# Kernel tuning notes

Measured on AMD Instinct MI355X. Metric: run time of the kernel, lower is better.

## Reference

```python
import jax, jax.numpy as jnp
import numpy as np

# ---- static part graph (matches torch.nonzero row-major edge order) ----
ADJ = np.array([[0,1,0,0,0,0],
                [1,0,1,1,1,1],
                [0,1,0,0,0,0],
                [0,1,0,0,0,0],
                [0,1,0,0,0,1],
                [0,1,0,0,1,0]], dtype=np.int64)
EDGES = [(int(u), int(v)) for u, v in np.argwhere(ADJ)]  # 12 edges
P = ADJ.shape[0]                 # 6 part nodes (cls_p - 1)
PART_LIST = [[] for _ in range(P)]
for u, v in EDGES:
    PART_LIST[v].append(u)
DEG = [len(l) for l in PART_LIST]  # [1,5,1,1,2,2], sum = 12
CLS_P = P + 1
IN_DIM, HID = 256, 10
N, H, W = 4, 64, 64


def spatial_coords(h, w):
    """[8,h,w] coord features, same as generate_spatial_batch (vectorized)."""
    ws = np.arange(w, dtype=np.float32); hs = np.arange(h, dtype=np.float32)
    xmin = ws / w * 2 - 1; xmax = (ws + 1) / w * 2 - 1; xctr = (xmin + xmax) / 2
    ymin = hs / h * 2 - 1; ymax = (hs + 1) / h * 2 - 1; yctr = (ymin + ymax) / 2
    f = np.zeros((h, w, 8), np.float32)
    f[..., 0] = xmin[None, :]; f[..., 1] = ymin[:, None]
    f[..., 2] = xmax[None, :]; f[..., 3] = ymax[:, None]
    f[..., 4] = xctr[None, :]; f[..., 5] = yctr[:, None]
    f[..., 6] = 1.0 / w;       f[..., 7] = 1.0 / h
    return jnp.asarray(f.transpose(2, 0, 1))


def conv1x1(x, w, b=None):
    y = jnp.einsum('nchw,oc->nohw', x, w)
    return y if b is None else y + b[None, :, None, None]


def conv3x3(x, w):
    return jax.lax.conv_general_dilated(x, w, (1, 1), 'SAME',
                                        dimension_numbers=('NCHW', 'OIHW', 'NCHW'))


def bn(x, g, b, eps=1e-5):
    mu = x.mean((0, 2, 3), keepdims=True)
    var = ((x - mu) ** 2).mean((0, 2, 3), keepdims=True)
    return (x - mu) * jax.lax.rsqrt(var + eps) * g[None, :, None, None] + b[None, :, None, None]


def setup_inputs() -> dict:
    key = jax.random.key(0)
    ks = jax.random.split(key, 16)
    s = 0.05
    return {
        'xp':      jax.random.normal(ks[0], (N, IN_DIM, H, W), jnp.float32),
        'p_nodes': jax.random.normal(ks[1], (CLS_P, N, HID, H, W), jnp.float32),
        'p_atts':  jax.random.normal(ks[2], (CLS_P, N, 1, H, W), jnp.float32),
        'W_key':  jax.random.normal(ks[3], (64, IN_DIM + 8), jnp.float32) * s,
        'b_key':  jnp.zeros((64,), jnp.float32),
        'W_q':    jax.random.normal(ks[4], (64, IN_DIM + 8), jnp.float32) * s,
        'b_q':    jnp.zeros((64,), jnp.float32),
        'W_att':  jax.random.normal(ks[5], (sum(DEG), IN_DIM + 1), jnp.float32) * s,
        'b_att':  jnp.zeros((sum(DEG),), jnp.float32),
        'W_proj': jax.random.normal(ks[6], (HID, IN_DIM), jnp.float32) * s,
        'g_proj': jnp.ones((HID,), jnp.float32),
        'bt_proj': jnp.zeros((HID,), jnp.float32),
        'W_rel1': jax.random.normal(ks[7], (2 * HID, 2 * HID, 3, 3), jnp.float32) * s,
        'g_rel1': jnp.ones((2 * HID,), jnp.float32),
        'bt_rel1': jnp.zeros((2 * HID,), jnp.float32),
        'W_rel2': jax.random.normal(ks[8], (HID, 2 * HID), jnp.float32) * s,
        'b_rel2': jnp.zeros((HID,), jnp.float32),
        'Wg':    jax.random.normal(ks[9], (P, 2, 2 * HID), jnp.float32) * s,
        'bg':    jnp.zeros((P, 2), jnp.float32),
        'Wc':    jax.random.normal(ks[10], (P, HID, 2 * HID), jnp.float32) * s,
        'g_can': jnp.ones((P, HID), jnp.float32),
        'bt_can': jnp.zeros((P, HID), jnp.float32),
    }


def reference(xp, p_nodes, p_atts,
              W_key, b_key, W_q, b_q, W_att, b_att,
              W_proj, g_proj, bt_proj, W_rel1, g_rel1, bt_rel1, W_rel2, b_rel2,
              Wg, bg, Wc, g_can, bt_can):
    n, c, h, w = xp.shape
    L = h * w
    coord = jnp.broadcast_to(spatial_coords(h, w), (n, 8, h, w))

    # ---- Dep_Context (vectorized over the P part nodes) ----
    feat = jnp.concatenate([xp, coord], axis=1)                 # [n, 264, h, w]
    key_f = conv1x1(feat, W_key, b_key).reshape(n, 64, L)       # [n, 64, L]
    p_att = p_atts[1:]                                          # [P, n, 1, h, w]
    norm = jax.nn.softmax(p_att.reshape(P, n, L), axis=-1)      # [P, n, L]
    hu_c = jnp.einsum('ncl,pnl->pnc', xp.reshape(n, c, L), norm)       # [P, n, 256]
    co_c = jnp.einsum('ncl,pnl->pnc', coord.reshape(n, 8, L), norm)    # [P, n, 8]
    cen = jnp.concatenate([hu_c, co_c], axis=-1)                # [P, n, 264]
    q = jnp.einsum('pnf,of->pno', cen, W_q) + b_q               # [P, n, 64]
    energy = jnp.einsum('pno,nol->pnl', q, key_f)               # [P, n, L]
    attn = jax.nn.sigmoid(energy).reshape(P, n, 1, h, w)
    one_m = 1.0 - p_att
    F_dep_att = attn * one_m                                    # [P, n, 1, h, w]
    F_dep = attn * xp[None] * one_m                             # [P, n, 256, h, w]

    # ---- Contexture attention heads (per-node conv, deg_i output channels) ----
    att_logits, att_soft = [], []
    off = 0
    for i in range(P):
        d = DEG[i]
        inp = jnp.concatenate([F_dep_att[i], xp], axis=1)       # [n, 257, h, w]
        logit = conv1x1(inp, W_att[off:off + d], b_att[off:off + d])
        att_logits.append(logit)
        att_soft.append(jax.nn.softmax(logit, axis=1))
        off += d

    # ---- Dependency messages per edge ----
    def dependency(hv, hu_ctx, dep_att):
        msg = jax.nn.relu(bn(conv1x1(hu_ctx * dep_att, W_proj), g_proj, bt_proj))
        x = jnp.concatenate([msg, hv], axis=1)                  # [n, 20, h, w]
        x = jax.nn.relu(bn(conv3x3(x, W_rel1), g_rel1, bt_rel1))
        return jax.nn.sigmoid(conv1x1(x, W_rel2, b_rel2))       # [n, 10, h, w]

    msgs = [None] * P
    for u, v in EDGES:
        ch = PART_LIST[u].index(v)
        # NB: original code indexes p_node_list with the raw edge target v
        m = dependency(p_nodes[v], F_dep[u], att_soft[u][:, ch:ch + 1])
        msgs[v] = m if msgs[v] is None else msgs[v] + m

    # ---- ConvGRU node updates ----
    new_nodes = [p_nodes[0]]
    for i in range(P):
        h_cur, msg = p_nodes[i + 1], msgs[i]
        gates = conv1x1(jnp.concatenate([msg, h_cur], axis=1), Wg[i], bg[i])
        r = jax.nn.sigmoid(gates[:, 0:1]); z = jax.nn.sigmoid(gates[:, 1:2])
        cnm = conv1x1(jnp.concatenate([msg, r * h_cur], axis=1), Wc[i])
        cnm = jax.nn.leaky_relu(bn(cnm, g_can[i], bt_can[i]), 0.01)  # InPlaceABNSync default
        new_nodes.append((1.0 - z) * h_cur + z * cnm)

    xp_new = jnp.stack(new_nodes)                               # [cls_p, n, 10, h, w]
    fdep_att = jnp.concatenate(att_logits, axis=1)              # [n, 12, h, w]
    return xp_new, fdep_att
```

## Files before the change

### kernel.cpp

```cpp
#include <hip/hip_runtime.h>
#include <math.h>

#define L 4096

__constant__ int c_EV[12]   = {1,0,2,3,4,5,1,1,1,5,1,4};
__constant__ int c_INOFF[7] = {0,1,6,7,8,10,12};
__constant__ int c_INE[12]  = {1, 0,6,7,8,10, 2, 3, 4,11, 5,9};

__device__ inline float sigmf(float x){ return 1.f/(1.f+expf(-x)); }

__global__ __launch_bounds__(256) void k_softmax_norm(const float* __restrict__ p_atts,
                                                      float* __restrict__ norm){
  int pn = blockIdx.x;
  const float* src = p_atts + (size_t)(pn + 4) * L;
  float* dst = norm + (size_t)pn * L;
  __shared__ float red[256];
  int tid = threadIdx.x;
  float m = -1e30f;
  for (int l = tid; l < L; l += 256) m = fmaxf(m, src[l]);
  red[tid] = m; __syncthreads();
  for (int s = 128; s; s >>= 1){ if (tid < s) red[tid] = fmaxf(red[tid], red[tid+s]); __syncthreads(); }
  m = red[0]; __syncthreads();
  float sum = 0.f;
  for (int l = tid; l < L; l += 256) sum += expf(src[l] - m);
  red[tid] = sum; __syncthreads();
  for (int s = 128; s; s >>= 1){ if (tid < s) red[tid] += red[tid+s]; __syncthreads(); }
  float inv = 1.f / red[0];
  for (int l = tid; l < L; l += 256) dst[l] = expf(src[l] - m) * inv;
}

__device__ inline float coord_feat(int cc, int l){
  int h = l >> 6, w = l & 63;
  const float s = 2.f / 64.f;
  switch (cc){
    case 0: return w * s - 1.f;
    case 1: return h * s - 1.f;
    case 2: return (w + 1) * s - 1.f;
    case 3: return (h + 1) * s - 1.f;
    case 4: return (w + 0.5f) * s - 1.f;
    case 5: return (h + 0.5f) * s - 1.f;
    default: return 1.f / 64.f;
  }
}

__global__ __launch_bounds__(256) void k_centroid(const float* __restrict__ xp,
                                                  const float* __restrict__ norm,
                                                  float* __restrict__ cen){
  int c = blockIdx.x;
  int n = blockIdx.y;
  int tid = threadIdx.x;
  float acc[6];
#pragma unroll
  for (int p = 0; p < 6; p++) acc[p] = 0.f;
  const float* nr0 = norm + (size_t)n * L;
  if (c < 256){
    const float* xr = xp + ((size_t)n * 256 + c) * L;
    for (int l = tid; l < L; l += 256){
      float xv = xr[l];
#pragma unroll
      for (int p = 0; p < 6; p++) acc[p] = fmaf(xv, nr0[(size_t)p * 4 * L + l], acc[p]);
    }
  } else {
    int cc = c - 256;
    for (int l = tid; l < L; l += 256){
      float xv = coord_feat(cc, l);
#pragma unroll
      for (int p = 0; p < 6; p++) acc[p] = fmaf(xv, nr0[(size_t)p * 4 * L + l], acc[p]);
    }
  }
#pragma unroll
  for (int p = 0; p < 6; p++){
    for (int off = 32; off; off >>= 1) acc[p] += __shfl_xor(acc[p], off, 64);
  }
  __shared__ float red[6][4];
  int wv = tid >> 6;
  if ((tid & 63) == 0){
#pragma unroll
    for (int p = 0; p < 6; p++) red[p][wv] = acc[p];
  }
  __syncthreads();
  if (tid < 6){
    float s = red[tid][0] + red[tid][1] + red[tid][2] + red[tid][3];
    cen[(size_t)(tid * 4 + n) * 264 + c] = s;
  }
}

__global__ __launch_bounds__(256) void k_qk(const float* __restrict__ cen,
                                            const float* __restrict__ W_q, const float* __restrict__ b_q,
                                            const float* __restrict__ W_key, const float* __restrict__ b_key,
                                            float* __restrict__ qk, float* __restrict__ qb){
  int pn = blockIdx.x;
  int tid = threadIdx.x;
  __shared__ float cen_s[264];
  __shared__ float qs[64];
  __shared__ float part[256];
  for (int i = tid; i < 264; i += 256) cen_s[i] = cen[(size_t)pn * 264 + i];
  __syncthreads();
  int o = tid >> 2, pr = tid & 3;
  {
    float a = 0.f;
    int f0 = pr * 66;
    for (int j = 0; j < 66; j++){ int f = f0 + j; a = fmaf(cen_s[f], W_q[o * 264 + f], a); }
    part[tid] = a;
  }
  __syncthreads();
  if (pr == 0) qs[o] = part[tid] + part[tid + 1] + part[tid + 2] + part[tid + 3] + b_q[o];
  __syncthreads();
  for (int c = tid; c < 264; c += 256){
    float a = 0.f;
    for (int oo = 0; oo < 64; oo++) a = fmaf(qs[oo], W_key[oo * 264 + c], a);
    qk[(size_t)pn * 264 + c] = a;
  }
  if (tid < 64) part[tid] = qs[tid] * b_key[tid];
  __syncthreads();
  if (tid == 0){
    float a = 0.f;
    for (int oo = 0; oo < 64; oo++) a += part[oo];
    qb[pn] = a;
  }
}

__global__ __launch_bounds__(256) void k_wt(const float* __restrict__ W_rel1, float* __restrict__ wt2){
  for (int i = threadIdx.x; i < 3600; i += 256){
    int co = i % 10; int t = i / 10;
    int k = t % 9; t /= 9;
    int h = t & 1; int ci = t >> 1;
    wt2[i] = W_rel1[(((h * 10 + co) * 20) + ci) * 9 + k];
  }
}

__global__ __launch_bounds__(256) void k_pixel(const float* __restrict__ xp,
                                              const float* __restrict__ p_atts,
                                              const float* __restrict__ W_att, const float* __restrict__ b_att,
                                              const float* __restrict__ W_proj,
                                              const float* __restrict__ qk, const float* __restrict__ qb,
                                              float* __restrict__ out_fdep,
                                              float* __restrict__ s_edge,
                                              float* __restrict__ proj_x){
  __shared__ float s_watt[256 * 12];
  __shared__ float s_wproj[256 * 12];
  __shared__ float s_qk[256 * 8];
  __shared__ float s_qkt[48];
  __shared__ float pacc[4][28][64];
  __shared__ float w0[12], ba[12], qbs[6];
  int n = blockIdx.y;
  int tid = threadIdx.x;
  int wv = tid >> 6, w = tid & 63;
  int l = blockIdx.x * 64 + w;
  for (int i = tid; i < 256 * 12; i += 256){ int c = i / 12, j = i % 12; s_watt[i] = W_att[j * 257 + 1 + c]; }
  for (int i = tid; i < 256 * 12; i += 256){ int c = i / 12, k = i % 12; s_wproj[i] = (k < 10) ? W_proj[k * 256 + c] : 0.f; }
  for (int i = tid; i < 256 * 8; i += 256){ int c = i >> 3, p = i & 7; s_qk[i] = (p < 6) ? qk[((size_t)(p * 4 + n)) * 264 + c] : 0.f; }
  if (tid < 48){ int p = tid >> 3, cc = tid & 7; s_qkt[tid] = qk[((size_t)(p * 4 + n)) * 264 + 256 + cc]; }
  if (tid < 12){ w0[tid] = W_att[tid * 257]; ba[tid] = b_att[tid]; }
  if (tid < 6) qbs[tid] = qb[tid * 4 + n];
  __syncthreads();

  float a[32];
#pragma unroll
  for (int f = 0; f < 32; f++) a[f] = 0.f;
  const float* xpn = xp + (size_t)n * 256 * L + l;
  int c0 = wv * 64;
#pragma unroll 2
  for (int cc = 0; cc < 64; cc++){
    int c = c0 + cc;
    float xv = xpn[(size_t)c * L];
    float4 wa0 = *(const float4*)(s_watt + c * 12);
    float4 wa1 = *(const float4*)(s_watt + c * 12 + 4);
    float4 wa2 = *(const float4*)(s_watt + c * 12 + 8);
    float4 wp0 = *(const float4*)(s_wproj + c * 12);
    float4 wp1 = *(const float4*)(s_wproj + c * 12 + 4);
    float4 wp2 = *(const float4*)(s_wproj + c * 12 + 8);
    float4 wq0 = *(const float4*)(s_qk + c * 8);
    float4 wq1 = *(const float4*)(s_qk + c * 8 + 4);
    a[0]  = fmaf(xv, wa0.x, a[0]);  a[1]  = fmaf(xv, wa0.y, a[1]);
    a[2]  = fmaf(xv, wa0.z, a[2]);  a[3]  = fmaf(xv, wa0.w, a[3]);
    a[4]  = fmaf(xv, wa1.x, a[4]);  a[5]  = fmaf(xv, wa1.y, a[5]);
    a[6]  = fmaf(xv, wa1.z, a[6]);  a[7]  = fmaf(xv, wa1.w, a[7]);
    a[8]  = fmaf(xv, wa2.x, a[8]);  a[9]  = fmaf(xv, wa2.y, a[9]);
    a[10] = fmaf(xv, wa2.z, a[10]); a[11] = fmaf(xv, wa2.w, a[11]);
    a[12] = fmaf(xv, wp0.x, a[12]); a[13] = fmaf(xv, wp0.y, a[13]);
    a[14] = fmaf(xv, wp0.z, a[14]); a[15] = fmaf(xv, wp0.w, a[15]);
    a[16] = fmaf(xv, wp1.x, a[16]); a[17] = fmaf(xv, wp1.y, a[17]);
    a[18] = fmaf(xv, wp1.z, a[18]); a[19] = fmaf(xv, wp1.w, a[19]);
    a[20] = fmaf(xv, wp2.x, a[20]); a[21] = fmaf(xv, wp2.y, a[21]);
    a[24] = fmaf(xv, wq0.x, a[24]); a[25] = fmaf(xv, wq0.y, a[25]);
    a[26] = fmaf(xv, wq0.z, a[26]); a[27] = fmaf(xv, wq0.w, a[27]);
    a[28] = fmaf(xv, wq1.x, a[28]); a[29] = fmaf(xv, wq1.y, a[29]);
  }
#pragma unroll
  for (int f = 0; f < 12; f++) pacc[wv][f][w] = a[f];
#pragma unroll
  for (int k = 0; k < 10; k++) pacc[wv][12 + k][w] = a[12 + k];
#pragma unroll
  for (int p = 0; p < 6; p++) pacc[wv][22 + p][w] = a[24 + p];
  __syncthreads();
  for (int idx = tid; idx < 28 * 64; idx += 256){
    int f = idx >> 6, ww = idx & 63;
    pacc[0][f][ww] = pacc[0][f][ww] + pacc[1][f][ww] + pacc[2][f][ww] + pacc[3][f][ww];
  }
  __syncthreads();
  if (tid < 64){
    float accA[12], accP[10], accE[6];
#pragma unroll
    for (int j = 0; j < 12; j++) accA[j] = pacc[0][j][w];
#pragma unroll
    for (int k = 0; k < 10; k++) accP[k] = pacc[0][12 + k][w];
#pragma unroll
    for (int p = 0; p < 6; p++) accE[p] = pacc[0][22 + p][w];

    float cf[8];
    { int hh = l >> 6, ww2 = l & 63; const float s = 2.f / 64.f;
      cf[0] = ww2 * s - 1.f; cf[1] = hh * s - 1.f; cf[2] = (ww2 + 1) * s - 1.f; cf[3] = (hh + 1) * s - 1.f;
      cf[4] = (ww2 + 0.5f) * s - 1.f; cf[5] = (hh + 0.5f) * s - 1.f; cf[6] = 1.f / 64.f; cf[7] = 1.f / 64.f; }
    float sat[6];
#pragma unroll
    for (int p = 0; p < 6; p++){
      float e = accE[p] + qbs[p];
#pragma unroll
      for (int cc = 0; cc < 8; cc++) e = fmaf(cf[cc], s_qkt[p * 8 + cc], e);
      float aa = sigmf(e);
      float pa = p_atts[((size_t)(p + 1) * 4 + n) * L + l];
      sat[p] = aa * (1.f - pa);
    }
    const int part_of[12] = {0,1,1,1,1,1,2,3,4,4,5,5};
    float lg[12];
#pragma unroll
    for (int j = 0; j < 12; j++){
      lg[j] = accA[j] + w0[j] * sat[part_of[j]] + ba[j];
      out_fdep[((size_t)n * 12 + j) * L + l] = lg[j];
    }
    const int gs[6] = {0,1,6,7,8,10}, gd[6] = {1,5,1,1,2,2};
    float sm[12];
#pragma unroll
    for (int g = 0; g < 6; g++){
      int s0 = gs[g], d = gd[g];
      float mx = lg[s0];
      for (int t = 1; t < d; t++) mx = fmaxf(mx, lg[s0 + t]);
      float ssum = 0.f;
      for (int t = 0; t < d; t++){ float e2 = expf(lg[s0 + t] - mx); sm[s0 + t] = e2; ssum += e2; }
      float inv = 1.f / ssum;
      for (int t = 0; t < d; t++) sm[s0 + t] *= inv;
    }
#pragma unroll
    for (int e = 0; e < 12; e++) s_edge[((size_t)e * 4 + n) * L + l] = sat[part_of[e]] * sm[e];
#pragma unroll
    for (int k = 0; k < 10; k++) proj_x[((size_t)n * 10 + k) * L + l] = accP[k];
  }
}

__global__ __launch_bounds__(256) void k_msg_stats(const float* __restrict__ proj_x,
                                                   const float* __restrict__ s_edge,
                                                   float* __restrict__ mu, float* __restrict__ istd){
  int e = blockIdx.x / 10, k = blockIdx.x % 10;
  int tid = threadIdx.x;
  float s1 = 0.f, s2 = 0.f;
  for (int idx = tid; idx < 4 * L; idx += 256){
    int n = idx >> 12, l = idx & (L - 1);
    float t = proj_x[((size_t)n * 10 + k) * L + l] * s_edge[((size_t)e * 4 + n) * L + l];
    s1 += t; s2 += t * t;
  }
  __shared__ float r1[256], r2[256];
  r1[tid] = s1; r2[tid] = s2; __syncthreads();
  for (int s = 128; s; s >>= 1){ if (tid < s){ r1[tid] += r1[tid+s]; r2[tid] += r2[tid+s]; } __syncthreads(); }
  if (tid == 0){
    float m = r1[0] / 16384.f, v = r2[0] / 16384.f - m * m;
    mu[blockIdx.x] = m; istd[blockIdx.x] = rsqrtf(v + 1e-5f);
  }
}

__global__ __launch_bounds__(256) void k_conv3(const float* __restrict__ proj_x,
                                               const float* __restrict__ s_edge,
                                               const float* __restrict__ mu, const float* __restrict__ istd,
                                               const float* __restrict__ g_proj, const float* __restrict__ bt_proj,
                                               const float* __restrict__ p_nodes,
                                               const float* __restrict__ wt2,
                                               float* __restrict__ y,
                                               float* __restrict__ ypart){
  __shared__ float red[4][20];
  int rb = blockIdx.x, n = blockIdx.y;
  int e = blockIdx.z >> 1, h = blockIdx.z & 1;
  int v = c_EV[e];
  int tid = threadIdx.x;
  int wv = tid >> 6, w = tid & 63;
  int row = rb * 4 + wv;
  float mLm = (w == 0) ? 0.f : 1.f;
  float mRm = (w == 63) ? 0.f : 1.f;

  float scs[10], sbs[10];
#pragma unroll
  for (int k = 0; k < 10; k++){
    int ek = e * 10 + k;
    float s = istd[ek] * g_proj[k];
    scs[k] = s; sbs[k] = bt_proj[k] - mu[ek] * s;
  }
  const size_t enL = ((size_t)e * 4 + n) * L;
  const float* se = s_edge + enL;

  float acc[10];
#pragma unroll
  for (int co = 0; co < 10; co++) acc[co] = 0.f;

#pragma unroll 2
  for (int ci = 0; ci < 10; ci++){
    const float* pr = proj_x + ((size_t)n * 10 + ci) * L;
    float a = 0.f, b, c = 0.f;
    { int pix = row * 64 + w; float t = pr[pix] * se[pix]; b = fmaxf(fmaf(t, scs[ci], sbs[ci]), 0.f); }
    if (row > 0){ int pix = (row - 1) * 64 + w; float t = pr[pix] * se[pix]; a = fmaxf(fmaf(t, scs[ci], sbs[ci]), 0.f); }
    if (row < 63){ int pix = (row + 1) * 64 + w; float t = pr[pix] * se[pix]; c = fmaxf(fmaf(t, scs[ci], sbs[ci]), 0.f); }
    float aL = __shfl_up(a, 1) * mLm;
    float aR = __shfl_down(a, 1) * mRm;
    float bL = __shfl_up(b, 1) * mLm;
    float bR = __shfl_down(b, 1) * mRm;
    float cL = __shfl_up(c, 1) * mLm;
    float cR = __shfl_down(c, 1) * mRm;
    const float* wp = wt2 + (ci * 2 + h) * 90;
#pragma unroll
    for (int co = 0; co < 10; co++){
      float s0 = fmaf(aL, wp[co], fmaf(a, wp[10 + co], aR * wp[20 + co]));
      s0 = fmaf(bL, wp[30 + co], fmaf(b, wp[40 + co], fmaf(bR, wp[50 + co], s0)));
      s0 = fmaf(cL, wp[60 + co], fmaf(c, wp[70 + co], fmaf(cR, wp[80 + co], s0)));
      acc[co] += s0;
    }
  }
#pragma unroll 2
  for (int ci = 10; ci < 20; ci++){
    const float* pn = p_nodes + (((size_t)v * 4 + n) * 10 + (ci - 10)) * L;
    float a = 0.f, b, c = 0.f;
    b = pn[row * 64 + w];
    if (row > 0)  a = pn[(row - 1) * 64 + w];
    if (row < 63) c = pn[(row + 1) * 64 + w];
    float aL = __shfl_up(a, 1) * mLm;
    float aR = __shfl_down(a, 1) * mRm;
    float bL = __shfl_up(b, 1) * mLm;
    float bR = __shfl_down(b, 1) * mRm;
    float cL = __shfl_up(c, 1) * mLm;
    float cR = __shfl_down(c, 1) * mRm;
    const float* wp = wt2 + (ci * 2 + h) * 90;
#pragma unroll
    for (int co = 0; co < 10; co++){
      float s0 = fmaf(aL, wp[co], fmaf(a, wp[10 + co], aR * wp[20 + co]));
      s0 = fmaf(bL, wp[30 + co], fmaf(b, wp[40 + co], fmaf(bR, wp[50 + co], s0)));
      s0 = fmaf(cL, wp[60 + co], fmaf(c, wp[70 + co], fmaf(cR, wp[80 + co], s0)));
      acc[co] += s0;
    }
  }

  int ch0 = h * 10;
#pragma unroll
  for (int co = 0; co < 10; co++)
    y[(enL * 20) + ((size_t)(ch0 + co)) * L + row * 64 + w] = acc[co];

#pragma unroll
  for (int co = 0; co < 10; co++){
    float s1 = acc[co];
    float s2 = acc[co] * acc[co];
    for (int off = 32; off; off >>= 1){ s1 += __shfl_xor(s1, off, 64); s2 += __shfl_xor(s2, off, 64); }
    if (w == 0){ red[wv][2 * co] = s1; red[wv][2 * co + 1] = s2; }
  }
  __syncthreads();
  if (tid < 20){
    int co = tid >> 1, which = tid & 1;
    float s = red[0][tid] + red[1][tid] + red[2][tid] + red[3][tid];
    ypart[(((size_t)(e * 20 + ch0 + co) * 64) + n * 16 + rb) * 2 + which] = s;
  }
}

__global__ __launch_bounds__(64) void k_red(const float* __restrict__ part,
                                            float* __restrict__ mu, float* __restrict__ istd){
  int ent = blockIdx.x;
  int t = threadIdx.x;
  const float* p = part + ((size_t)ent * 64 + t) * 2;
  float s1 = p[0], s2 = p[1];
  for (int off = 32; off; off >>= 1){ s1 += __shfl_xor(s1, off, 64); s2 += __shfl_xor(s2, off, 64); }
  if (t == 0){
    float m = s1 / 16384.f, v = s2 / 16384.f - m * m;
    mu[ent] = m; istd[ent] = rsqrtf(v + 1e-5f);
  }
}

__global__ __launch_bounds__(256) void k_mout_gru(const float* __restrict__ y,
                                                  const float* __restrict__ mu_y, const float* __restrict__ istd_y,
                                                  const float* __restrict__ g_rel1, const float* __restrict__ bt_rel1,
                                                  const float* __restrict__ W_rel2, const float* __restrict__ b_rel2,
                                                  const float* __restrict__ p_nodes,
                                                  const float* __restrict__ Wg, const float* __restrict__ bg,
                                                  const float* __restrict__ Wc,
                                                  float* __restrict__ cnm, float* __restrict__ zbuf,
                                                  float* __restrict__ cpart){
  int i = blockIdx.z, n = blockIdx.y;
  int tid = threadIdx.x;
  int l = blockIdx.x * 256 + tid;
  __shared__ float w2[200], wc[200], wg[40], bgs[2];
  __shared__ float sc[5][20], sb[5][20];
  __shared__ float red[4][20];
  int ne = c_INOFF[i + 1] - c_INOFF[i];
  for (int t = tid; t < 200; t += 256){ w2[t] = W_rel2[t]; wc[t] = Wc[i * 200 + t]; }
  if (tid < 40) wg[tid] = Wg[i * 40 + tid];
  if (tid < 2) bgs[tid] = bg[i * 2 + tid];
  if (tid < ne * 20){
    int ei = tid / 20, c = tid % 20;
    int e = c_INE[c_INOFF[i] + ei];
    int ec = e * 20 + c;
    float s = istd_y[ec] * g_rel1[c];
    sc[ei][c] = s; sb[ei][c] = bt_rel1[c] - mu_y[ec] * s;
  }
  __syncthreads();
  float m[10];
#pragma unroll
  for (int k = 0; k < 10; k++) m[k] = 0.f;
  for (int ei = 0; ei < ne; ei++){
    int e = c_INE[c_INOFF[i] + ei];
    float z[20];
#pragma unroll
    for (int c = 0; c < 20; c++){
      float t = y[(((size_t)e * 4 + n) * 20 + c) * L + l];
      z[c] = fmaxf(t * sc[ei][c] + sb[ei][c], 0.f);
    }
#pragma unroll
    for (int k = 0; k < 10; k++){
      float a = b_rel2[k];
#pragma unroll
      for (int c = 0; c < 20; c++) a = fmaf(w2[k * 20 + c], z[c], a);
      m[k] += sigmf(a);
    }
  }
  float h[10];
#pragma unroll
  for (int k = 0; k < 10; k++) h[k] = p_nodes[(((size_t)(i + 1) * 4 + n) * 10 + k) * L + l];
  float g0 = bgs[0], g1 = bgs[1];
#pragma unroll
  for (int k = 0; k < 10; k++){
    g0 = fmaf(wg[k], m[k], g0); g0 = fmaf(wg[10 + k], h[k], g0);
    g1 = fmaf(wg[20 + k], m[k], g1); g1 = fmaf(wg[30 + k], h[k], g1);
  }
  float r = sigmf(g0), zz = sigmf(g1);
  zbuf[((size_t)i * 4 + n) * L + l] = zz;
  float cv[10];
#pragma unroll
  for (int k = 0; k < 10; k++){
    float a = 0.f;
#pragma unroll
    for (int c = 0; c < 10; c++){
      a = fmaf(wc[k * 20 + c], m[c], a);
      a = fmaf(wc[k * 20 + 10 + c], r * h[c], a);
    }
    cv[k] = a;
    cnm[(((size_t)i * 4 + n) * 10 + k) * L + l] = a;
  }
  int wv = tid >> 6, w = tid & 63;
#pragma unroll
  for (int k = 0; k < 10; k++){
    float s1 = cv[k], s2 = cv[k] * cv[k];
    for (int off = 32; off; off >>= 1){ s1 += __shfl_xor(s1, off, 64); s2 += __shfl_xor(s2, off, 64); }
    if (w == 0){ red[wv][2 * k] = s1; red[wv][2 * k + 1] = s2; }
  }
  __syncthreads();
  if (tid < 20){
    float s = red[0][tid] + red[1][tid] + red[2][tid] + red[3][tid];
    int k = tid >> 1, which = tid & 1;
    cpart[(((size_t)(i * 10 + k) * 64) + n * 16 + blockIdx.x) * 2 + which] = s;
  }
}

__global__ __launch_bounds__(256) void k_out(const float* __restrict__ cnm, const float* __restrict__ zbuf,
                                             const float* __restrict__ p_nodes,
                                             const float* __restrict__ mu, const float* __restrict__ istd,
                                             const float* __restrict__ g_can, const float* __restrict__ bt_can,
                                             float* __restrict__ out){
  int idx = blockIdx.x * 256 + threadIdx.x;
  const int NODE = 4 * 10 * L;
  if (idx < NODE){ out[idx] = p_nodes[idx]; return; }
  int j = idx - NODE;
  int l = j & (L - 1); int r = j >> 12;
  int k = r % 10; r /= 10; int n = r & 3; int i = r >> 2;
  int ik = i * 10 + k;
  float c = cnm[j];
  float cn = (c - mu[ik]) * istd[ik] * g_can[ik] + bt_can[ik];
  cn = cn > 0.f ? cn : 0.01f * cn;
  float z = zbuf[((size_t)i * 4 + n) * L + l];
  float h = p_nodes[idx];
  out[idx] = (1.f - z) * h + z * cn;
}

extern "C" void kernel_launch(void* const* d_in, const int* in_sizes, int n_in,
                              void* d_out, int out_size, void* d_ws, size_t ws_size,
                              hipStream_t stream){
  (void)in_sizes; (void)n_in; (void)out_size; (void)ws_size;
  const float* xp      = (const float*)d_in[0];
  const float* p_nodes = (const float*)d_in[1];
  const float* p_atts  = (const float*)d_in[2];
  const float* W_key   = (const float*)d_in[3];
  const float* b_key   = (const float*)d_in[4];
  const float* W_q     = (const float*)d_in[5];
  const float* b_q     = (const float*)d_in[6];
  const float* W_att   = (const float*)d_in[7];
  const float* b_att   = (const float*)d_in[8];
  const float* W_proj  = (const float*)d_in[9];
  const float* g_proj  = (const float*)d_in[10];
  const float* bt_proj = (const float*)d_in[11];
  const float* W_rel1  = (const float*)d_in[12];
  const float* g_rel1  = (const float*)d_in[13];
  const float* bt_rel1 = (const float*)d_in[14];
  const float* W_rel2  = (const float*)d_in[15];
  const float* b_rel2  = (const float*)d_in[16];
  const float* Wg      = (const float*)d_in[17];
  const float* bg      = (const float*)d_in[18];
  const float* Wc      = (const float*)d_in[19];
  const float* g_can   = (const float*)d_in[20];
  const float* bt_can  = (const float*)d_in[21];

  float* out      = (float*)d_out;
  float* fdep_out = out + (size_t)7 * 4 * 10 * L;

  float* w = (float*)d_ws;
  size_t off = 0;
  auto alloc = [&](size_t nf){ float* p = w + off; off += nf; return p; };
  float* norm    = alloc((size_t)6 * 4 * L);
  float* cen     = alloc(6 * 4 * 264);
  float* qk      = alloc(6 * 4 * 264);
  float* qb      = alloc(24);
  float* wt2     = alloc(3600);
  float* proj_x  = alloc((size_t)4 * 10 * L);
  float* s_edge  = alloc((size_t)12 * 4 * L);
  float* mu_msg  = alloc(120);
  float* istd_msg= alloc(120);
  float* ybuf    = alloc((size_t)12 * 4 * 20 * L);
  float* ypart   = alloc(240 * 64 * 2);
  float* cpart   = alloc(60 * 64 * 2);
  float* mu_y    = alloc(240);
  float* istd_y  = alloc(240);
  float* cnm     = alloc((size_t)6 * 4 * 10 * L);
  float* zbuf    = alloc((size_t)6 * 4 * L);
  float* mu_c    = alloc(60);
  float* istd_c  = alloc(60);

  k_wt<<<1, 256, 0, stream>>>(W_rel1, wt2);
  k_softmax_norm<<<24, 256, 0, stream>>>(p_atts, norm);
  { dim3 g(264, 4); k_centroid<<<g, 256, 0, stream>>>(xp, norm, cen); }
  k_qk<<<24, 256, 0, stream>>>(cen, W_q, b_q, W_key, b_key, qk, qb);
  { dim3 g(64, 4); k_pixel<<<g, 256, 0, stream>>>(xp, p_atts, W_att, b_att, W_proj, qk, qb, fdep_out, s_edge, proj_x); }
  k_msg_stats<<<120, 256, 0, stream>>>(proj_x, s_edge, mu_msg, istd_msg);
  { dim3 g(16, 4, 24); k_conv3<<<g, 256, 0, stream>>>(proj_x, s_edge, mu_msg, istd_msg, g_proj, bt_proj, p_nodes, wt2, ybuf, ypart); }
  k_red<<<240, 64, 0, stream>>>(ypart, mu_y, istd_y);
  { dim3 g(16, 4, 6); k_mout_gru<<<g, 256, 0, stream>>>(ybuf, mu_y, istd_y, g_rel1, bt_rel1, W_rel2, b_rel2,
                                                        p_nodes, Wg, bg, Wc, cnm, zbuf, cpart); }
  k_red<<<60, 64, 0, stream>>>(cpart, mu_c, istd_c);
  k_out<<<(7 * 4 * 10 * L) / 256, 256, 0, stream>>>(cnm, zbuf, p_nodes, mu_c, istd_c, g_can, bt_can, out);
}
```

Measured before the change: 162.8 us.

## Compute two output rows per thread in conv3 and fuse weight transpose kernel

The 3x3 conv kernel now has each thread produce two adjacent output rows, so it loads 4 input rows instead of 3 per output row and reuses every weight load across both rows. The grid's row-block dimension is halved and the partial-stats reduction now takes a variable part count. The separate weight-transpose kernel is folded into an extra block of the softmax kernel, removing one launch. Holding two accumulator sets raises register pressure and halves the number of blocks, which may reduce occupancy.

```diff
diff --git a/kernel.cpp b/kernel.cpp
--- a/kernel.cpp
+++ b/kernel.cpp
@@ -10,12 +10,23 @@
 __device__ inline float sigmf(float x){ return 1.f/(1.f+expf(-x)); }
 
 __global__ __launch_bounds__(256) void k_softmax_norm(const float* __restrict__ p_atts,
-                                                      float* __restrict__ norm){
+                                                      float* __restrict__ norm,
+                                                      const float* __restrict__ W_rel1,
+                                                      float* __restrict__ wt2){
+  int tid = threadIdx.x;
+  if (blockIdx.x == 24){
+    for (int i = tid; i < 3600; i += 256){
+      int co = i % 10; int t = i / 10;
+      int k = t % 9; t /= 9;
+      int h = t & 1; int ci = t >> 1;
+      wt2[i] = W_rel1[(((h * 10 + co) * 20) + ci) * 9 + k];
+    }
+    return;
+  }
   int pn = blockIdx.x;
   const float* src = p_atts + (size_t)(pn + 4) * L;
   float* dst = norm + (size_t)pn * L;
   __shared__ float red[256];
-  int tid = threadIdx.x;
   float m = -1e30f;
   for (int l = tid; l < L; l += 256) m = fmaxf(m, src[l]);
   red[tid] = m; __syncthreads();
@@ -117,15 +128,6 @@
     float a = 0.f;
     for (int oo = 0; oo < 64; oo++) a += part[oo];
     qb[pn] = a;
-  }
-}
-
-__global__ __launch_bounds__(256) void k_wt(const float* __restrict__ W_rel1, float* __restrict__ wt2){
-  for (int i = threadIdx.x; i < 3600; i += 256){
-    int co = i % 10; int t = i / 10;
-    int k = t % 9; t /= 9;
-    int h = t & 1; int ci = t >> 1;
-    wt2[i] = W_rel1[(((h * 10 + co) * 20) + ci) * 9 + k];
   }
 }
 
@@ -282,7 +284,7 @@
   int v = c_EV[e];
   int tid = threadIdx.x;
   int wv = tid >> 6, w = tid & 63;
-  int row = rb * 4 + wv;
+  int r0 = rb * 8 + wv * 2;
   float mLm = (w == 0) ? 0.f : 1.f;
   float mRm = (w == 63) ? 0.f : 1.f;
 
@@ -295,65 +297,87 @@
   }
   const size_t enL = ((size_t)e * 4 + n) * L;
   const float* se = s_edge + enL;
-
-  float acc[10];
-#pragma unroll
-  for (int co = 0; co < 10; co++) acc[co] = 0.f;
-
-#pragma unroll 2
+  float se4[4];
+#pragma unroll
+  for (int j = 0; j < 4; j++){
+    int rr = r0 - 1 + j;
+    se4[j] = (rr >= 0 && rr < 64) ? se[rr * 64 + w] : 0.f;
+  }
+
+  float acc0[10], acc1[10];
+#pragma unroll
+  for (int co = 0; co < 10; co++){ acc0[co] = 0.f; acc1[co] = 0.f; }
+
   for (int ci = 0; ci < 10; ci++){
     const float* pr = proj_x + ((size_t)n * 10 + ci) * L;
-    float a = 0.f, b, c = 0.f;
-    { int pix = row * 64 + w; float t = pr[pix] * se[pix]; b = fmaxf(fmaf(t, scs[ci], sbs[ci]), 0.f); }
-    if (row > 0){ int pix = (row - 1) * 64 + w; float t = pr[pix] * se[pix]; a = fmaxf(fmaf(t, scs[ci], sbs[ci]), 0.f); }
-    if (row < 63){ int pix = (row + 1) * 64 + w; float t = pr[pix] * se[pix]; c = fmaxf(fmaf(t, scs[ci], sbs[ci]), 0.f); }
-    float aL = __shfl_up(a, 1) * mLm;
-    float aR = __shfl_down(a, 1) * mRm;
-    float bL = __shfl_up(b, 1) * mLm;
-    float bR = __shfl_down(b, 1) * mRm;
-    float cL = __shfl_up(c, 1) * mLm;
-    float cR = __shfl_down(c, 1) * mRm;
+    float mC[4];
+#pragma unroll
+    for (int j = 0; j < 4; j++){
+      int rr = r0 - 1 + j;
+      if (rr >= 0 && rr < 64){
+        float t = pr[rr * 64 + w] * se4[j];
+        mC[j] = fmaxf(fmaf(t, scs[ci], sbs[ci]), 0.f);
+      } else mC[j] = 0.f;
+    }
+    float mL[4], mR[4];
+#pragma unroll
+    for (int j = 0; j < 4; j++){
+      mL[j] = __shfl_up(mC[j], 1) * mLm;
+      mR[j] = __shfl_down(mC[j], 1) * mRm;
+    }
     const float* wp = wt2 + (ci * 2 + h) * 90;
 #pragma unroll
-    for (int co = 0; co < 10; co++){
-      float s0 = fmaf(aL, wp[co], fmaf(a, wp[10 + co], aR * wp[20 + co]));
-      s0 = fmaf(bL, wp[30 + co], fmaf(b, wp[40 + co], fmaf(bR, wp[50 + co], s0)));
-      s0 = fmaf(cL, wp[60 + co], fmaf(c, wp[70 + co], fmaf(cR, wp[80 + co], s0)));
-      acc[co] += s0;
-    }
-  }
-#pragma unroll 2
+    for (int ky = 0; ky < 3; ky++){
+#pragma unroll
+      for (int co = 0; co < 10; co++){
+        float w0v = wp[(ky * 3 + 0) * 10 + co];
+        float w1v = wp[(ky * 3 + 1) * 10 + co];
+        float w2v = wp[(ky * 3 + 2) * 10 + co];
+        acc0[co] = fmaf(mL[ky], w0v, fmaf(mC[ky], w1v, fmaf(mR[ky], w2v, acc0[co])));
+        acc1[co] = fmaf(mL[ky + 1], w0v, fmaf(mC[ky + 1], w1v, fmaf(mR[ky + 1], w2v, acc1[co])));
+      }
+    }
+  }
   for (int ci = 10; ci < 20; ci++){
-    const float* pn = p_nodes + (((size_t)v * 4 + n) * 10 + (ci - 10)) * L;
-    float a = 0.f, b, c = 0.f;
-    b = pn[row * 64 + w];
-    if (row > 0)  a = pn[(row - 1) * 64 + w];
-    if (row < 63) c = pn[(row + 1) * 64 + w];
-    float aL = __shfl_up(a, 1) * mLm;
-    float aR = __shfl_down(a, 1) * mRm;
-    float bL = __shfl_up(b, 1) * mLm;
-    float bR = __shfl_down(b, 1) * mRm;
-    float cL = __shfl_up(c, 1) * mLm;
-    float cR = __shfl_down(c, 1) * mRm;
+    const float* pnp = p_nodes + (((size_t)v * 4 + n) * 10 + (ci - 10)) * L;
+    float mC[4];
+#pragma unroll
+    for (int j = 0; j < 4; j++){
+      int rr = r0 - 1 + j;
+      mC[j] = (rr >= 0 && rr < 64) ? pnp[rr * 64 + w] : 0.f;
+    }
+    float mL[4], mR[4];
+#pragma unroll
+    for (int j = 0; j < 4; j++){
+      mL[j] = __shfl_up(mC[j], 1) * mLm;
+      mR[j] = __shfl_down(mC[j], 1) * mRm;
+    }
     const float* wp = wt2 + (ci * 2 + h) * 90;
 #pragma unroll
-    for (int co = 0; co < 10; co++){
-      float s0 = fmaf(aL, wp[co], fmaf(a, wp[10 + co], aR * wp[20 + co]));
-      s0 = fmaf(bL, wp[30 + co], fmaf(b, wp[40 + co], fmaf(bR, wp[50 + co], s0)));
-      s0 = fmaf(cL, wp[60 + co], fmaf(c, wp[70 + co], fmaf(cR, wp[80 + co], s0)));
-      acc[co] += s0;
+    for (int ky = 0; ky < 3; ky++){
+#pragma unroll
+      for (int co = 0; co < 10; co++){
+        float w0v = wp[(ky * 3 + 0) * 10 + co];
+        float w1v = wp[(ky * 3 + 1) * 10 + co];
+        float w2v = wp[(ky * 3 + 2) * 10 + co];
+        acc0[co] = fmaf(mL[ky], w0v, fmaf(mC[ky], w1v, fmaf(mR[ky], w2v, acc0[co])));
+        acc1[co] = fmaf(mL[ky + 1], w0v, fmaf(mC[ky + 1], w1v, fmaf(mR[ky + 1], w2v, acc1[co])));
+      }
     }
   }
 
   int ch0 = h * 10;
 #pragma unroll
-  for (int co = 0; co < 10; co++)
-    y[(enL * 20) + ((size_t)(ch0 + co)) * L + row * 64 + w] = acc[co];
-
-#pragma unroll
   for (int co = 0; co < 10; co++){
-    float s1 = acc[co];
-    float s2 = acc[co] * acc[co];
+    size_t base = enL * 20 + ((size_t)(ch0 + co)) * L;
+    y[base + r0 * 64 + w] = acc0[co];
+    y[base + (r0 + 1) * 64 + w] = acc1[co];
+  }
+
+#pragma unroll
+  for (int co = 0; co < 10; co++){
+    float s1 = acc0[co] + acc1[co];
+    float s2 = acc0[co] * acc0[co] + acc1[co] * acc1[co];
     for (int off = 32; off; off >>= 1){ s1 += __shfl_xor(s1, off, 64); s2 += __shfl_xor(s2, off, 64); }
     if (w == 0){ red[wv][2 * co] = s1; red[wv][2 * co + 1] = s2; }
   }
@@ -361,16 +385,19 @@
   if (tid < 20){
     int co = tid >> 1, which = tid & 1;
     float s = red[0][tid] + red[1][tid] + red[2][tid] + red[3][tid];
-    ypart[(((size_t)(e * 20 + ch0 + co) * 64) + n * 16 + rb) * 2 + which] = s;
-  }
-}
-
-__global__ __launch_bounds__(64) void k_red(const float* __restrict__ part,
+    ypart[(((size_t)(e * 20 + ch0 + co) * 32) + n * 8 + rb) * 2 + which] = s;
+  }
+}
+
+__global__ __launch_bounds__(64) void k_red(const float* __restrict__ part, int npart,
                                             float* __restrict__ mu, float* __restrict__ istd){
   int ent = blockIdx.x;
   int t = threadIdx.x;
-  const float* p = part + ((size_t)ent * 64 + t) * 2;
-  float s1 = p[0], s2 = p[1];
+  float s1 = 0.f, s2 = 0.f;
+  if (t < npart){
+    const float* p = part + ((size_t)ent * npart + t) * 2;
+    s1 = p[0]; s2 = p[1];
+  }
   for (int off = 32; off; off >>= 1){ s1 += __shfl_xor(s1, off, 64); s2 += __shfl_xor(s2, off, 64); }
   if (t == 0){
     float m = s1 / 16384.f, v = s2 / 16384.f - m * m;
@@ -525,7 +552,7 @@
   float* mu_msg  = alloc(120);
   float* istd_msg= alloc(120);
   float* ybuf    = alloc((size_t)12 * 4 * 20 * L);
-  float* ypart   = alloc(240 * 64 * 2);
+  float* ypart   = alloc(240 * 32 * 2);
   float* cpart   = alloc(60 * 64 * 2);
   float* mu_y    = alloc(240);
   float* istd_y  = alloc(240);
@@ -534,16 +561,15 @@
   float* mu_c    = alloc(60);
   float* istd_c  = alloc(60);
 
-  k_wt<<<1, 256, 0, stream>>>(W_rel1, wt2);
-  k_softmax_norm<<<24, 256, 0, stream>>>(p_atts, norm);
+  k_softmax_norm<<<25, 256, 0, stream>>>(p_atts, norm, W_rel1, wt2);
   { dim3 g(264, 4); k_centroid<<<g, 256, 0, stream>>>(xp, norm, cen); }
   k_qk<<<24, 256, 0, stream>>>(cen, W_q, b_q, W_key, b_key, qk, qb);
   { dim3 g(64, 4); k_pixel<<<g, 256, 0, stream>>>(xp, p_atts, W_att, b_att, W_proj, qk, qb, fdep_out, s_edge, proj_x); }
   k_msg_stats<<<120, 256, 0, stream>>>(proj_x, s_edge, mu_msg, istd_msg);
-  { dim3 g(16, 4, 24); k_conv3<<<g, 256, 0, stream>>>(proj_x, s_edge, mu_msg, istd_msg, g_proj, bt_proj, p_nodes, wt2, ybuf, ypart); }
-  k_red<<<240, 64, 0, stream>>>(ypart, mu_y, istd_y);
+  { dim3 g(8, 4, 24); k_conv3<<<g, 256, 0, stream>>>(proj_x, s_edge, mu_msg, istd_msg, g_proj, bt_proj, p_nodes, wt2, ybuf, ypart); }
+  k_red<<<240, 64, 0, stream>>>(ypart, 32, mu_y, istd_y);
   { dim3 g(16, 4, 6); k_mout_gru<<<g, 256, 0, stream>>>(ybuf, mu_y, istd_y, g_rel1, bt_rel1, W_rel2, b_rel2,
                                                         p_nodes, Wg, bg, Wc, cnm, zbuf, cpart); }
-  k_red<<<60, 64, 0, stream>>>(cpart, mu_c, istd_c);
+  k_red<<<60, 64, 0, stream>>>(cpart, 64, mu_c, istd_c);
   k_out<<<(7 * 4 * 10 * L) / 256, 256, 0, stream>>>(cnm, zbuf, p_nodes, mu_c, istd_c, g_can, bt_can, out);
 }
```

Result: faster. 152.0 us (-6.6%).
